# Optimization experiments

Hardware: AMD Instinct MI355X
Metric: run time of the kernel (lower is better)

Reference implementation:

```python
import jax, jax.numpy as jnp
import numpy as np

BN_EPS = 1e-5


def setup_inputs() -> dict:
    key = jax.random.key(0)
    ks = jax.random.split(key, 10)
    B, C, Ci, H, W = 4, 256, 128, 64, 64
    s = 0.05
    return {
        "x": jax.random.normal(ks[0], (B, C, H, W), jnp.float32),
        "g_w": jax.random.normal(ks[1], (Ci, C), jnp.float32) * s,
        "g_b": jax.random.normal(ks[2], (Ci,), jnp.float32) * s,
        "theta_w": jax.random.normal(ks[3], (Ci, C), jnp.float32) * s,
        "theta_b": jax.random.normal(ks[4], (Ci,), jnp.float32) * s,
        "phi_w": jax.random.normal(ks[5], (Ci, C), jnp.float32) * s,
        "phi_b": jax.random.normal(ks[6], (Ci,), jnp.float32) * s,
        "W_w": jax.random.normal(ks[7], (C, Ci), jnp.float32) * s,
        "W_b": jax.random.normal(ks[8], (C,), jnp.float32) * s,
        "bn_gamma": jnp.ones((C,), jnp.float32),
        "bn_beta": jnp.zeros((C,), jnp.float32),
        "scale": jax.random.normal(ks[9], (1,), jnp.float32),
    }


def reference(x, g_w, g_b, theta_w, theta_b, phi_w, phi_b, W_w, W_b, bn_gamma, bn_beta, scale):
    B, C, H, W = x.shape
    xf = x.reshape(B, C, H * W)  # [B, C, N]
    # 1x1 conv projections == channel matmuls
    g = jnp.einsum('oc,bcn->bno', g_w, xf) + g_b            # [B, N, Ci]
    th = jnp.einsum('oc,bcn->bno', theta_w, xf) + theta_b   # [B, N, Ci]
    ph = jnp.einsum('oc,bcn->bon', phi_w, xf) + phi_b[:, None]  # [B, Ci, N]
    # unscaled attention: f = theta @ phi, softmax over keys
    f = jnp.einsum('bnd,bdm->bnm', th, ph)                  # [B, N, N]
    attn = jax.nn.softmax(f, axis=-1)
    y = jnp.einsum('bnm,bmo->bno', attn, g)                 # [B, N, Ci]
    y4 = y.transpose(0, 2, 1).reshape(B, -1, H, W)          # [B, Ci, H, W]
    # W: 1x1 conv + BatchNorm2d (training mode: batch statistics)
    wy = jnp.einsum('od,bdhw->bohw', W_w, y4) + W_b[None, :, None, None]
    mean = wy.mean(axis=(0, 2, 3))
    var = wy.var(axis=(0, 2, 3))
    bn = (wy - mean[None, :, None, None]) * jax.lax.rsqrt(var[None, :, None, None] + BN_EPS)
    bn = bn * bn_gamma[None, :, None, None] + bn_beta[None, :, None, None]
    return scale * bn + x
```

## Files before the change

### kernel.cpp

```cpp
#include <hip/hip_runtime.h>
#include <hip/hip_bf16.h>

#define BB 4
#define CC 256
#define CI 128
#define NN 4096

typedef _Float16 f16;
typedef __attribute__((ext_vector_type(8))) _Float16 f16x8;
typedef __attribute__((ext_vector_type(4))) float f32x4;

#define MFMA(a,b,c) __builtin_amdgcn_mfma_f32_16x16x32_f16(a,b,c,0,0,0)
#define LDS3(p) ((__attribute__((address_space(3))) void*)(p))
#define GL1(p)  ((const __attribute__((address_space(1))) void*)(p))

#define DPP_MAX(x, ctrl) { int _s=__float_as_int(x); \
    float _y=__int_as_float(__builtin_amdgcn_update_dpp(_s,_s,ctrl,0xF,0xF,false)); \
    x = fmaxf(x,_y); }
#define DPP_ADD(x, ctrl) { int _s=__float_as_int(x); \
    float _y=__int_as_float(__builtin_amdgcn_update_dpp(_s,_s,ctrl,0xF,0xF,false)); \
    x = x+_y; }
__device__ __forceinline__ float rowmax16(float x){
    DPP_MAX(x,0xB1) DPP_MAX(x,0x4E) DPP_MAX(x,0x141) DPP_MAX(x,0x140) return x;
}
__device__ __forceinline__ float rowsum16(float x){
    DPP_ADD(x,0xB1) DPP_ADD(x,0x4E) DPP_ADD(x,0x141) DPP_ADD(x,0x140) return x;
}

__global__ __launch_bounds__(256) void k01_xpose(const float* x, f16* xt,
                                                 const float* tw, const float* pw,
                                                 const float* gw, const float* Ww, f16* wdst){
    int nt = blockIdx.x, ct = blockIdx.y, b = blockIdx.z;
    __shared__ float tile[64][65];
    int t = threadIdx.x;
    const float* src = x + ((size_t)(b*CC + ct*64))*NN + nt*64;
    #pragma unroll
    for (int k=0;k<16;k++){ int idx=t+k*256; int cl=idx>>6, nl=idx&63;
        tile[cl][nl]=src[(size_t)cl*NN + nl]; }
    __syncthreads();
    f16* dst = xt + ((size_t)(b*NN + nt*64))*CC + ct*64;
    #pragma unroll
    for (int k=0;k<16;k++){ int idx=t+k*256; int nl=idx>>6, cl=idx&63;
        dst[(size_t)nl*CC + cl] = (f16)tile[cl][nl]; }
    if (t < 128){
        int blkId = blockIdx.x + 64*(blockIdx.y + 4*blockIdx.z);
        int i = blkId*128 + t;
        int j = i & 32767; int sel = i >> 15;
        const float* s = (sel==0)? tw : (sel==1)? pw : (sel==2)? gw : Ww;
        wdst[i] = (f16)s[j];
    }
}

__global__ __launch_bounds__(256) void k2_all(const f16* xt, const f16* thw, const f16* phw,
                                              const f16* gwh, const float* thb, const float* phb,
                                              const float* gb, f16* th, f16* ph, f16* gt2){
    int b = blockIdx.y; int xx = blockIdx.x;
    int wv = threadIdx.x>>6, lane = threadIdx.x&63, q=lane>>4, cc=lane&15;
    if (xx < 64){
        int mat = xx>>5; int ntile = xx&31;
        int n0 = ntile*128 + wv*32;
        f16x8 aq[2][8];
        #pragma unroll
        for (int ns=0;ns<2;ns++){
            const f16* ap = xt + ((size_t)(b*NN + n0 + ns*16 + cc))*CC + q*8;
            #pragma unroll
            for (int kk=0;kk<8;kk++) aq[ns][kk] = *(const f16x8*)(ap + kk*32);
        }
        const f16* w   = mat? phw : thw;
        const float* bias = mat? phb : thb;
        f16* o = mat? ph : th;
        #pragma unroll 1
        for (int os=0;os<8;os++){
            f32x4 acc0={0,0,0,0}, acc1={0,0,0,0};
            const f16* wp = w + ((size_t)(os*16 + cc))*CC + q*8;
            #pragma unroll
            for (int kk=0;kk<8;kk++){
                f16x8 bf = *(const f16x8*)(wp + kk*32);
                acc0 = MFMA(aq[0][kk], bf, acc0);
                acc1 = MFMA(aq[1][kk], bf, acc1);
            }
            float bv = bias[os*16+cc];
            #pragma unroll
            for (int r=0;r<4;r++){
                o[((size_t)(b*NN + n0      + 4*q + r))*CI + os*16 + cc] = (f16)(acc0[r] + bv);
                o[((size_t)(b*NN + n0 + 16 + 4*q + r))*CI + os*16 + cc] = (f16)(acc1[r] + bv);
            }
        }
    } else {
        int mt = xx - 64;
        f16x8 ag[2][8];
        #pragma unroll
        for (int os=0;os<2;os++){
            const f16* ap = gwh + ((size_t)(wv*32 + os*16 + cc))*CC + q*8;
            #pragma unroll
            for (int kk=0;kk<8;kk++) ag[os][kk] = *(const f16x8*)(ap + kk*32);
        }
        f32x4 acc[2][4];
        #pragma unroll
        for (int os=0;os<2;os++){
            #pragma unroll
            for (int ms=0;ms<4;ms++) acc[os][ms]=(f32x4){0,0,0,0};
        }
        #pragma unroll 1
        for (int kk=0;kk<8;kk++){
            #pragma unroll
            for (int ms=0;ms<4;ms++){
                f16x8 bf = *(const f16x8*)(xt + ((size_t)(b*NN + mt*64 + ms*16 + cc))*CC + kk*32 + q*8);
                acc[0][ms]=MFMA(ag[0][kk],bf,acc[0][ms]);
                acc[1][ms]=MFMA(ag[1][kk],bf,acc[1][ms]);
            }
        }
        #pragma unroll
        for (int os=0;os<2;os++){
            #pragma unroll
            for (int r=0;r<4;r++){
                int orow = wv*32 + os*16 + 4*q + r;
                float bv = gb[orow];
                #pragma unroll
                for (int ms=0;ms<4;ms++)
                    gt2[((size_t)(b*64 + mt))*8192 + orow*64 + ms*16 + cc] = (f16)(acc[os][ms][r] + bv);
            }
        }
    }
}

__global__ __launch_bounds__(256, 4) void k3_attn(const f16* th, const f16* ph, const f16* gt2,
                                                  f16* ypart, float* ml){
    int qt = blockIdx.x;
    int sp = blockIdx.y;
    int b  = blockIdx.z;
    int wv=threadIdx.x>>6, lane=threadIdx.x&63, q=lane>>4, cc=lane&15;
    int qrow0 = qt*64 + wv*16;
    int kv0 = sp*1024;
    int sw  = (cc&7)<<4;
    int sw2 = ((cc>>1)&3)<<4;

    __shared__ __align__(16) char ldsb[36864];
    char* phL = ldsb;
    char* gtL = ldsb + 16384;
    char* plw = ldsb + 32768 + wv*1024;

    f16x8 aq[4];
    const f16* thp = th + ((size_t)(b*NN + qrow0 + cc))*CI + q*8;
    #pragma unroll
    for (int kk=0;kk<4;kk++) aq[kk] = *(const f16x8*)(thp + kk*32);

    const char* phg = (const char*)(ph + (size_t)b*NN*CI);
    const char* gtg = (const char*)gt2 + (size_t)b*64*16384;

    f32x4 yacc[8];
    #pragma unroll
    for (int os=0;os<8;os++) yacc[os]=(f32x4){0,0,0,0};
    float m_run[4];
    f32x4 l_vec=(f32x4){0,0,0,0};
    #pragma unroll
    for (int r=0;r<4;r++) m_run[r]=-1e30f;

    auto STAGE = [&](int tt, int bb){
        int key0 = kv0 + tt*32;
        int mt  = key0 >> 6;
        int kob = (key0 & 32)*2;
        char* pbase = phL + bb*8192 + wv*2048;
        char* gbase = gtL + bb*8192 + wv*2048;
        #pragma unroll
        for (int ch=0; ch<2; ch++){
            int prow = wv*8 + ch*4 + (lane>>4);
            const char* ps = phg + (size_t)(key0 + prow)*256 + (((lane&15)*16) ^ ((prow&7)<<4));
            __builtin_amdgcn_global_load_lds(GL1(ps), LDS3(pbase + ch*1024), 16, 0, 0);
            int gf = wv*2048 + ch*1024 + lane*16;
            int grow = gf>>6, gcol = gf&63;
            const char* gs = gtg + (size_t)mt*16384 + grow*128 + kob + (gcol ^ (((grow>>1)&3)<<4));
            __builtin_amdgcn_global_load_lds(GL1(gs), LDS3(gbase + ch*1024), 16, 0, 0);
        }
    };

    STAGE(0, 0);
    __syncthreads();

    int cur = 0;
    #pragma unroll 1
    for (int it=0; it<32; ++it){
        if (it < 31) STAGE(it+1, cur^1);
        const char* pt  = phL + cur*8192;
        const char* gtt = gtL + cur*8192;
        f32x4 fa[2];
        #pragma unroll
        for (int j=0;j<2;j++){
            f16x8 pf[4];
            #pragma unroll
            for (int kk=0;kk<4;kk++)
                pf[kk] = *(const f16x8*)(pt + (j*16+cc)*256 + ((kk*64 + q*16) ^ sw));
            fa[j]=(f32x4){0,0,0,0};
            #pragma unroll
            for (int kk=0;kk<4;kk++)
                fa[j]=MFMA(aq[kk], pf[kk], fa[j]);
        }
        float mx[4]; float need = 0.f;
        #pragma unroll
        for (int r=0;r<4;r++){
            float m0 = fmaxf(fa[0][r],fa[1][r]);
            m0 = rowmax16(m0);
            mx[r]=m0;
            need = fmaxf(need, m0 - m_run[r]);
        }
        if (__any(need > 3.f)){
            #pragma unroll
            for (int r=0;r<4;r++){
                float nm = fmaxf(m_run[r], mx[r]);
                float co = __expf(m_run[r]-nm);
                m_run[r]=nm;
                l_vec[r]*=co;
                #pragma unroll
                for (int os=0;os<8;os++) yacc[os][r]*=co;
            }
        }
        #pragma unroll
        for (int j=0;j<2;j++){
            #pragma unroll
            for (int r=0;r<4;r++) fa[j][r]=__expf(fa[j][r]-m_run[r]);
        }
        #pragma unroll
        for (int r=0;r<4;r++)
            l_vec[r] += fa[0][r]+fa[1][r];
        #pragma unroll
        for (int j=0;j<2;j++){
            #pragma unroll
            for (int r=0;r<4;r++){
                int R = 4*q+r;
                *(f16*)(plw + R*64 + (((j*16+cc)*2) ^ (((R>>1)&3)<<4))) = (f16)fa[j][r];
            }
        }
        {
            f16x8 pa0 = *(const f16x8*)(plw + cc*64 + ((q*16) ^ sw2));
            #pragma unroll
            for (int os=0;os<8;os++){
                f16x8 gv = *(const f16x8*)(gtt + (os*16+cc)*64 + ((q*16) ^ sw2));
                yacc[os] = MFMA(pa0, gv, yacc[os]);
            }
        }
        __syncthreads();
        cur ^= 1;
    }
    float linv[4], lred[4];
    #pragma unroll
    for (int r=0;r<4;r++){
        float l = rowsum16(l_vec[r]);
        lred[r]=l; linv[r]=1.f/l;
    }
    #pragma unroll
    for (int os=0;os<8;os++){
        #pragma unroll
        for (int r=0;r<4;r++)
            ypart[((size_t)((sp*4+b)*NN + qrow0 + 4*q + r))*CI + os*16 + cc] = (f16)(yacc[os][r]*linv[r]);
    }
    if (cc==0){
        #pragma unroll
        for (int r=0;r<4;r++){
            size_t row = (size_t)(sp*4+b)*NN + qrow0 + 4*q + r;
            ml[row*2]   = m_run[r];
            ml[row*2+1] = lred[r];
        }
    }
}

__global__ __launch_bounds__(256) void k3c(const f16* ypart, const float* ml,
                                           f16* y, float* part, float* mupart){
    int blk = blockIdx.x; int t = threadIdx.x;
    int rloc = t>>2;
    int row  = blk*64 + rloc;
    int b = row>>12, n = row & 4095;
    int o0 = (t&3)*32;
    __shared__ __align__(16) f16 ldsT[128*64];
    float m_s[4], l_s[4];
    #pragma unroll
    for (int s=0;s<4;s++){ size_t r2 = ((size_t)(s*4+b)*NN + n)*2; m_s[s]=ml[r2]; l_s[s]=ml[r2+1]; }
    float M = fmaxf(fmaxf(m_s[0],m_s[1]),fmaxf(m_s[2],m_s[3]));
    float w[4]; float L=0.f;
    #pragma unroll
    for (int s=0;s<4;s++){ w[s]=l_s[s]*__expf(m_s[s]-M); L+=w[s]; }
    float inv = 1.f/L;
    #pragma unroll
    for (int s=0;s<4;s++) w[s]*=inv;
    float acc[32];
    #pragma unroll
    for (int j=0;j<32;j++) acc[j]=0.f;
    #pragma unroll
    for (int s=0;s<4;s++){
        const f16* src = ypart + ((size_t)(s*4+b)*NN + n)*CI + o0;
        #pragma unroll
        for (int v=0;v<4;v++){
            f16x8 vv = *(const f16x8*)(src + v*8);
            #pragma unroll
            for (int e=0;e<8;e++) acc[v*8+e] += w[s]*(float)vv[e];
        }
    }
    f16* yo = y + (size_t)row*CI + o0;
    #pragma unroll
    for (int v=0;v<4;v++){
        f16x8 ov;
        #pragma unroll
        for (int e=0;e<8;e++) ov[e] = (f16)acc[v*8+e];
        *(f16x8*)(yo + v*8) = ov;
        #pragma unroll
        for (int e=0;e<8;e++){
            int o = o0 + v*8 + e;
            ldsT[o*64 + (rloc ^ ((o&7)<<3))] = ov[e];
        }
    }
    __syncthreads();
    int wv=t>>6, lane=t&63, q=lane>>4, cc=lane&15;
    f32x4 gacc[2][8];
    #pragma unroll
    for (int a=0;a<2;a++)
        #pragma unroll
        for (int c2=0;c2<8;c2++) gacc[a][c2]=(f32x4){0,0,0,0};
    f16x8 af[2][2];
    #pragma unroll
    for (int o1t=0;o1t<2;o1t++){
        int o1 = (wv*2+o1t)*16+cc;
        #pragma unroll
        for (int kk=0;kk<2;kk++)
            af[o1t][kk] = *(const f16x8*)(ldsT + o1*64 + ((kk*32+q*8) ^ ((o1&7)<<3)));
    }
    #pragma unroll 1
    for (int o2t=0;o2t<8;o2t++){
        int o2 = o2t*16+cc;
        #pragma unroll
        for (int kk=0;kk<2;kk++){
            f16x8 bf = *(const f16x8*)(ldsT + o2*64 + ((kk*32+q*8) ^ ((o2&7)<<3)));
            gacc[0][o2t] = MFMA(af[0][kk], bf, gacc[0][o2t]);
            gacc[1][o2t] = MFMA(af[1][kk], bf, gacc[1][o2t]);
        }
    }
    float* pb = part + (size_t)blk*16384;
    #pragma unroll
    for (int o1t=0;o1t<2;o1t++){
        #pragma unroll
        for (int o2t=0;o2t<8;o2t++){
            #pragma unroll
            for (int r=0;r<4;r++)
                pb[((wv*2+o1t)*16+4*q+r)*128 + o2t*16+cc] = gacc[o1t][o2t][r];
        }
    }
    if (t<128){
        float sm=0.f;
        #pragma unroll
        for (int v=0;v<8;v++){
            f16x8 vv = *(const f16x8*)(ldsT + t*64 + ((v*8) ^ ((t&7)<<3)));
            #pragma unroll
            for (int e=0;e<8;e++) sm += (float)vv[e];
        }
        mupart[blk*128 + t] = sm;
    }
}

__global__ __launch_bounds__(256) void k4b_red(const float* part, const float* mupart, float* S){
    int pc = blockIdx.y;
    int t = threadIdx.x;
    if (blockIdx.x < 64){
        int i = blockIdx.x*256 + t;
        float s=0.f;
        #pragma unroll 1
        for (int p=pc*32; p<pc*32+32; p++) s += part[(size_t)p*16384 + i];
        atomicAdd(&S[i], s);
    } else if (t < 128){
        float s=0.f;
        #pragma unroll 1
        for (int p=pc*32; p<pc*32+32; p++) s += mupart[p*128 + t];
        atomicAdd(&S[16384+t], s);
    }
}

__global__ __launch_bounds__(128) void k4c_coef(const float* S, const float* Ww, const float* Wb,
                                                const float* gamma, const float* beta,
                                                const float* scale, float* AB){
    int ch = blockIdx.x; int t = threadIdx.x;
    const float* w = Ww + ch*CI;
    float tmp=0.f;
    const float* Srow = S + t*CI;
    #pragma unroll 1
    for (int o2=0;o2<CI;o2++) tmp += Srow[o2]*w[o2];
    float v  = w[t]*tmp;
    float mc = w[t]*S[16384 + t];
    #pragma unroll
    for (int s=1;s<64;s<<=1){ v += __shfl_xor(v,s); mc += __shfl_xor(mc,s); }
    __shared__ float red[4];
    if ((t&63)==0){ red[(t>>6)*2]=v; red[(t>>6)*2+1]=mc; }
    __syncthreads();
    if (t==0){
        float wSw = red[0]+red[2];
        float wmu = red[1]+red[3];
        const float M = 16384.f;
        float meanwy = wmu/M + Wb[ch];
        float var = wSw/M - (wmu/M)*(wmu/M);
        float inv = rsqrtf(var + 1e-5f);
        float sc = scale[0];
        float A  = sc*gamma[ch]*inv;
        float B3 = sc*(beta[ch] - meanwy*inv*gamma[ch]);
        AB[ch]     = A;
        AB[256+ch] = B3 + A*Wb[ch];
    }
}

__global__ __launch_bounds__(256) void k5_out(const f16* Wwh, const f16* y, const float* x,
                                              const float* AB, float* out){
    int ntile = blockIdx.x;
    int cht   = blockIdx.y;
    int b     = blockIdx.z;
    int wv=threadIdx.x>>6, lane=threadIdx.x&63, q=lane>>4, cc=lane&15;
    int ch0 = cht*64 + wv*16;
    f16x8 aw[4];
    const f16* wp = Wwh + ((size_t)(ch0+cc))*CI + q*8;
    #pragma unroll
    for (int kk=0;kk<4;kk++) aw[kk]=*(const f16x8*)(wp+kk*32);
    float Ar[4], Br[4];
    #pragma unroll
    for (int r=0;r<4;r++){ Ar[r]=AB[ch0+4*q+r]; Br[r]=AB[256+ch0+4*q+r]; }
    #pragma unroll 1
    for (int ns=0;ns<8;ns++){
        int n0 = ntile*128 + ns*16;
        f32x4 acc={0,0,0,0};
        const f16* yp = y + ((size_t)(b*NN + n0 + cc))*CI + q*8;
        #pragma unroll
        for (int kk=0;kk<4;kk++) acc = MFMA(aw[kk], *(const f16x8*)(yp+kk*32), acc);
        #pragma unroll
        for (int r=0;r<4;r++){
            size_t addr = ((size_t)(b*CC + ch0 + 4*q + r))*NN + n0 + cc;
            out[addr] = x[addr] + Ar[r]*acc[r] + Br[r];
        }
    }
}

extern "C" void kernel_launch(void* const* d_in, const int* in_sizes, int n_in,
                              void* d_out, int out_size, void* d_ws, size_t ws_size,
                              hipStream_t stream){
    const float* x    = (const float*)d_in[0];
    const float* g_w  = (const float*)d_in[1];
    const float* g_b  = (const float*)d_in[2];
    const float* th_w = (const float*)d_in[3];
    const float* th_b = (const float*)d_in[4];
    const float* ph_w = (const float*)d_in[5];
    const float* ph_b = (const float*)d_in[6];
    const float* W_w  = (const float*)d_in[7];
    const float* W_b  = (const float*)d_in[8];
    const float* bg   = (const float*)d_in[9];
    const float* bb   = (const float*)d_in[10];
    const float* sc   = (const float*)d_in[11];

    char* ws = (char*)d_ws;
    f16* xt  = (f16*)(ws);
    f16* th  = (f16*)(ws + 8388608);
    f16* ph  = (f16*)(ws + 8388608 + 1*4194304);
    f16* gt2 = (f16*)(ws + 8388608 + 2*4194304);
    f16* y   = (f16*)(ws + 8388608 + 3*4194304);
    f16* wh  = (f16*)(ws + 8388608 + 4*4194304);
    float* ml    = (float*)(ws + 25427968);
    f16*   ypart = (f16*)(ws + 25952256);
    float* mupart= (float*)(ws + 42729472);
    float* part  = (float*)ws;
    float* S    = (float*)(ws + 42860544);
    float* AB   = (float*)(ws + 42926592);
    f16* th_wh = wh;
    f16* ph_wh = wh + 32768;
    f16* g_wh  = wh + 65536;
    f16* Ww_h  = wh + 98304;

    hipMemsetAsync(S, 0, 16512*sizeof(float), stream);
    hipLaunchKernelGGL(k01_xpose, dim3(64,4,4), dim3(256), 0, stream, x, xt, th_w, ph_w, g_w, W_w, wh);
    hipLaunchKernelGGL(k2_all,   dim3(128,4),   dim3(256), 0, stream, xt, th_wh, ph_wh, g_wh,
                       th_b, ph_b, g_b, th, ph, gt2);
    hipLaunchKernelGGL(k3_attn,  dim3(64,4,4),  dim3(256), 0, stream, th, ph, gt2, ypart, ml);
    hipLaunchKernelGGL(k3c,      dim3(256),     dim3(256), 0, stream, ypart, ml, y, part, mupart);
    hipLaunchKernelGGL(k4b_red,  dim3(65,8),    dim3(256), 0, stream, part, mupart, S);
    hipLaunchKernelGGL(k4c_coef, dim3(256),     dim3(128), 0, stream, S, W_w, W_b, bg, bb, sc, AB);
    hipLaunchKernelGGL(k5_out,   dim3(32,4,4),  dim3(256), 0, stream, Ww_h, y, x, AB, (float*)d_out);
}
```

Baseline: 162.8 us.

## Transpose attention MFMA operands to keep P in registers, dropping LDS round-trip

Swaps the A/B operands of the QK^T MFMA so each lane holds scores for a single query column. Row max and sum then need only two cross-lane shuffles instead of DPP row reductions over four rows. The exponentiated P tile is packed straight into an MFMA operand register rather than written to and reread from per-wave LDS, which removes the P staging buffer and shrinks LDS. The output is transposed through LDS so ypart is written with 16-byte vector stores. In exchange, the G-tile reads become split 8-byte LDS loads, and correctness depends on the new swizzled layout indexing.

```diff
diff --git a/kernel.cpp b/kernel.cpp
--- a/kernel.cpp
+++ b/kernel.cpp
@@ -8,24 +8,12 @@
 
 typedef _Float16 f16;
 typedef __attribute__((ext_vector_type(8))) _Float16 f16x8;
+typedef __attribute__((ext_vector_type(4))) _Float16 f16x4;
 typedef __attribute__((ext_vector_type(4))) float f32x4;
 
 #define MFMA(a,b,c) __builtin_amdgcn_mfma_f32_16x16x32_f16(a,b,c,0,0,0)
 #define LDS3(p) ((__attribute__((address_space(3))) void*)(p))
 #define GL1(p)  ((const __attribute__((address_space(1))) void*)(p))
-
-#define DPP_MAX(x, ctrl) { int _s=__float_as_int(x); \
-    float _y=__int_as_float(__builtin_amdgcn_update_dpp(_s,_s,ctrl,0xF,0xF,false)); \
-    x = fmaxf(x,_y); }
-#define DPP_ADD(x, ctrl) { int _s=__float_as_int(x); \
-    float _y=__int_as_float(__builtin_amdgcn_update_dpp(_s,_s,ctrl,0xF,0xF,false)); \
-    x = x+_y; }
-__device__ __forceinline__ float rowmax16(float x){
-    DPP_MAX(x,0xB1) DPP_MAX(x,0x4E) DPP_MAX(x,0x141) DPP_MAX(x,0x140) return x;
-}
-__device__ __forceinline__ float rowsum16(float x){
-    DPP_ADD(x,0xB1) DPP_ADD(x,0x4E) DPP_ADD(x,0x141) DPP_ADD(x,0x140) return x;
-}
 
 __global__ __launch_bounds__(256) void k01_xpose(const float* x, f16* xt,
                                                  const float* tw, const float* pw,
@@ -135,10 +123,9 @@
     int sw  = (cc&7)<<4;
     int sw2 = ((cc>>1)&3)<<4;
 
-    __shared__ __align__(16) char ldsb[36864];
+    __shared__ __align__(16) char ldsb[32768];
     char* phL = ldsb;
     char* gtL = ldsb + 16384;
-    char* plw = ldsb + 32768 + wv*1024;
 
     f16x8 aq[4];
     const f16* thp = th + ((size_t)(b*NN + qrow0 + cc))*CI + q*8;
@@ -151,10 +138,8 @@
     f32x4 yacc[8];
     #pragma unroll
     for (int os=0;os<8;os++) yacc[os]=(f32x4){0,0,0,0};
-    float m_run[4];
-    f32x4 l_vec=(f32x4){0,0,0,0};
-    #pragma unroll
-    for (int r=0;r<4;r++) m_run[r]=-1e30f;
+    float m_run = -1e30f;
+    float l_run = 0.f;
 
     auto STAGE = [&](int tt, int bb){
         int key0 = kv0 + tt*32;
@@ -193,73 +178,68 @@
             fa[j]=(f32x4){0,0,0,0};
             #pragma unroll
             for (int kk=0;kk<4;kk++)
-                fa[j]=MFMA(aq[kk], pf[kk], fa[j]);
-        }
-        float mx[4]; float need = 0.f;
-        #pragma unroll
-        for (int r=0;r<4;r++){
-            float m0 = fmaxf(fa[0][r],fa[1][r]);
-            m0 = rowmax16(m0);
-            mx[r]=m0;
-            need = fmaxf(need, m0 - m_run[r]);
-        }
-        if (__any(need > 3.f)){
-            #pragma unroll
-            for (int r=0;r<4;r++){
-                float nm = fmaxf(m_run[r], mx[r]);
-                float co = __expf(m_run[r]-nm);
-                m_run[r]=nm;
-                l_vec[r]*=co;
-                #pragma unroll
-                for (int os=0;os<8;os++) yacc[os][r]*=co;
-            }
+                fa[j]=MFMA(pf[kk], aq[kk], fa[j]);
+        }
+        float t0 = fmaxf(fmaxf(fa[0][0],fa[0][1]), fmaxf(fa[0][2],fa[0][3]));
+        float t1 = fmaxf(fmaxf(fa[1][0],fa[1][1]), fmaxf(fa[1][2],fa[1][3]));
+        float m0 = fmaxf(t0,t1);
+        m0 = fmaxf(m0, __shfl_xor(m0,16));
+        m0 = fmaxf(m0, __shfl_xor(m0,32));
+        if (__any(m0 - m_run > 3.f)){
+            float nm = fmaxf(m_run, m0);
+            float co = __expf(m_run - nm);
+            m_run = nm;
+            l_run *= co;
+            #pragma unroll
+            for (int os=0;os<8;os++) yacc[os] *= co;
         }
         #pragma unroll
         for (int j=0;j<2;j++){
             #pragma unroll
-            for (int r=0;r<4;r++) fa[j][r]=__expf(fa[j][r]-m_run[r]);
-        }
-        #pragma unroll
-        for (int r=0;r<4;r++)
-            l_vec[r] += fa[0][r]+fa[1][r];
-        #pragma unroll
-        for (int j=0;j<2;j++){
-            #pragma unroll
-            for (int r=0;r<4;r++){
-                int R = 4*q+r;
-                *(f16*)(plw + R*64 + (((j*16+cc)*2) ^ (((R>>1)&3)<<4))) = (f16)fa[j][r];
-            }
-        }
-        {
-            f16x8 pa0 = *(const f16x8*)(plw + cc*64 + ((q*16) ^ sw2));
-            #pragma unroll
-            for (int os=0;os<8;os++){
-                f16x8 gv = *(const f16x8*)(gtt + (os*16+cc)*64 + ((q*16) ^ sw2));
-                yacc[os] = MFMA(pa0, gv, yacc[os]);
-            }
+            for (int r=0;r<4;r++) fa[j][r] = __expf(fa[j][r]-m_run);
+        }
+        l_run += ((fa[0][0]+fa[0][1])+(fa[0][2]+fa[0][3]))
+               + ((fa[1][0]+fa[1][1])+(fa[1][2]+fa[1][3]));
+        f16x8 pb;
+        #pragma unroll
+        for (int r=0;r<4;r++){ pb[r]=(f16)fa[0][r]; pb[4+r]=(f16)fa[1][r]; }
+        #pragma unroll
+        for (int os=0;os<8;os++){
+            int row = os*16 + cc;
+            f16x4 lo = *(const f16x4*)(gtt + row*64 + (( 8*q)     ^ sw2));
+            f16x4 hi = *(const f16x4*)(gtt + row*64 + ((32 + 8*q) ^ sw2));
+            f16x8 ga;
+            #pragma unroll
+            for (int e=0;e<4;e++){ ga[e]=lo[e]; ga[4+e]=hi[e]; }
+            yacc[os] = MFMA(ga, pb, yacc[os]);
         }
         __syncthreads();
         cur ^= 1;
     }
-    float linv[4], lred[4];
-    #pragma unroll
-    for (int r=0;r<4;r++){
-        float l = rowsum16(l_vec[r]);
-        lred[r]=l; linv[r]=1.f/l;
-    }
+    float l = l_run;
+    l += __shfl_xor(l,16);
+    l += __shfl_xor(l,32);
+    float linv = 1.f/l;
+    f16* yl = (f16*)(ldsb + wv*4096);
     #pragma unroll
     for (int os=0;os<8;os++){
         #pragma unroll
-        for (int r=0;r<4;r++)
-            ypart[((size_t)((sp*4+b)*NN + qrow0 + 4*q + r))*CI + os*16 + cc] = (f16)(yacc[os][r]*linv[r]);
-    }
-    if (cc==0){
-        #pragma unroll
         for (int r=0;r<4;r++){
-            size_t row = (size_t)(sp*4+b)*NN + qrow0 + 4*q + r;
-            ml[row*2]   = m_run[r];
-            ml[row*2+1] = lred[r];
-        }
+            int o = os*16 + 4*q + r;
+            *(f16*)((char*)yl + cc*256 + ((o*2) ^ ((cc&7)<<4))) = (f16)(yacc[os][r]*linv);
+        }
+    }
+    #pragma unroll
+    for (int p=0;p<4;p++){
+        int idx = p*512 + lane*8;
+        int row = idx>>7, o0 = idx&127;
+        f16x8 v = *(const f16x8*)((char*)yl + row*256 + ((o0*2) ^ ((row&7)<<4)));
+        *(f16x8*)(ypart + ((size_t)((sp*4+b)*NN + qrow0 + row))*CI + o0) = v;
+    }
+    if (lane < 16){
+        size_t row = (size_t)(sp*4+b)*NN + qrow0 + lane;
+        ml[row*2]   = m_run;
+        ml[row*2+1] = l;
     }
 }
 
```

Result: faster. 155.9 us (-4.2%).
